# Kernel optimization log

Hardware: AMD Instinct MI355X
Metric: run time of the kernel (lower is better)

The kernel has to match this reference:

```python
import jax, jax.numpy as jnp
import numpy as np

N, E = 50000, 800000
IN, H, D = 64, 4, 16          # in_feats, num_heads, head_size (IN == H*D -> identity skip)
NT, ET = 2, 2                 # num node / edge types


def setup_inputs() -> dict:
    key = jax.random.key(0)
    ks = jax.random.split(key, 13)
    s = 0.05
    return {
        "x": jax.random.normal(ks[0], (N, IN), jnp.float32),
        # TypedLinear weights: one [in,out] matrix per node type (DGL TypedLinear, no bias)
        "Wk": jax.random.normal(ks[1], (NT, IN, H * D), jnp.float32) * s,
        "Wq": jax.random.normal(ks[2], (NT, IN, H * D), jnp.float32) * s,
        "Wv": jax.random.normal(ks[3], (NT, IN, H * D), jnp.float32) * s,
        "Wa": jax.random.normal(ks[4], (NT, H * D, H * D), jnp.float32) * s,
        # per-head, per-edge-type relation matrices (relation_att / relation_msg)
        "Ratt": jax.random.normal(ks[5], (H, ET, D, D), jnp.float32) * s,
        "Rmsg": jax.random.normal(ks[6], (H, ET, D, D), jnp.float32) * s,
        "pri": jnp.ones((H, ET), jnp.float32),   # relation_pri
        "skip": jnp.ones((NT,), jnp.float32),    # skip gate per node type
        "ntype": jax.random.randint(ks[7], (N,), 0, NT),
        "etype": jax.random.randint(ks[8], (E,), 0, ET),
        "src": jax.random.randint(ks[9], (E,), 0, N),
        "dst": jax.random.randint(ks[10], (E,), 0, N),
    }


def _typed_linear(x, W, types):
    # x:[N,I], W:[T,I,O], types:[N] -> y[n] = x[n] @ W[types[n]]
    # T is tiny (2): compute all types densely, then select per node.
    y_all = jnp.einsum('ni,tio->tno', x, W)
    return y_all[types, jnp.arange(x.shape[0])]


def reference(x, Wk, Wq, Wv, Wa, Ratt, Rmsg, pri, skip, ntype, etype, src, dst):
    n = x.shape[0]
    k = _typed_linear(x, Wk, ntype).reshape(n, H, D)
    q = _typed_linear(x, Wq, ntype).reshape(n, H, D)
    v = _typed_linear(x, Wv, ntype).reshape(n, H, D)
    # relation transforms per edge type, computed once at node level (ET is tiny),
    # then gathered per edge: equivalent to per-edge TypedLinear in DGL's message fn.
    katt = jnp.einsum('nhd,htdf->thnf', k, Ratt)   # [ET,H,N,D]
    vmsg = jnp.einsum('nhd,htdf->thnf', v, Rmsg)   # [ET,H,N,D]
    kw = katt[etype, :, src]                       # [E,H,D]
    m = vmsg[etype, :, src]                        # [E,H,D]
    qd = q[dst]                                    # [E,H,D]
    # attention logits: (K W_att) . Q * relation_pri / sqrt(d)
    a = (kw * qd).sum(-1) * pri[:, etype].T / jnp.sqrt(jnp.float32(D))  # [E,H]
    # edge softmax over incoming edges of each destination node (stable)
    amax = jax.ops.segment_max(a, dst, num_segments=n)                  # [N,H]
    ae = jnp.exp(a - amax[dst])
    asum = jax.ops.segment_sum(ae, dst, num_segments=n)
    attn = ae / asum[dst]                                               # [E,H]
    # scatter-aggregate messages
    h = jax.ops.segment_sum(m * attn[:, :, None], dst, num_segments=n)  # [N,H,D]
    # target-specific output projection (dropout is identity in eval)
    h = _typed_linear(h.reshape(n, H * D), Wa, ntype)                   # [N,H*D]
    # sigmoid-gated skip (in_feats == H*D so identity residual)
    alpha = jax.nn.sigmoid(skip)[ntype][:, None]
    return h * alpha + x * (1.0 - alpha)
```

## Files before the change

kernel.cpp:

```cpp
#include <hip/hip_runtime.h>
#include <math.h>
#include <stdint.h>

#define N_NODES 50000
#define N_EDGES 800000
#define NT_TYPES 2
#define ET_TYPES 2
#define NB_SCAN ((N_NODES + 255) / 256)
#define M_COLS 320
#define M_PER_T (64 * M_COLS)
#define PROJ_GRID ((N_NODES + 63) / 64)
#define SCAT_GRID ((N_EDGES + 1023) / 1024)
#define AGG_GRID ((N_NODES + 15) / 16)
#define MAXDEG 64
#define LOG2E 1.44269504088896f
#define HSTRIDE 36

typedef __attribute__((ext_vector_type(8))) short short8v;
typedef __attribute__((ext_vector_type(4))) float float4v;

__device__ __forceinline__ unsigned int f32_to_bf16(float f) {
  unsigned int u = __float_as_uint(f);
  return (u + 0x7FFFu + ((u >> 16) & 1u)) >> 16;
}

__device__ __forceinline__ float row16_sum(float p) {
  int r;
  r = __builtin_amdgcn_update_dpp(0, __float_as_int(p), 0x128, 0xf, 0xf, false);
  p += __int_as_float(r);
  r = __builtin_amdgcn_update_dpp(0, __float_as_int(p), 0x124, 0xf, 0xf, false);
  p += __int_as_float(r);
  r = __builtin_amdgcn_update_dpp(0, __float_as_int(p), 0x122, 0xf, 0xf, false);
  p += __int_as_float(r);
  r = __builtin_amdgcn_update_dpp(0, __float_as_int(p), 0x121, 0xf, 0xf, false);
  p += __int_as_float(r);
  return p;
}

__global__ void zero_kernel(int* __restrict__ deg) {
  const int i = blockIdx.x * 256 + threadIdx.x;
  if (i < N_NODES + 2) deg[i] = 0;
}

__global__ void prep_kernel(
    const float* __restrict__ Wk, const float* __restrict__ Wq,
    const float* __restrict__ Wv, const float* __restrict__ Wa,
    const float* __restrict__ Ratt, const float* __restrict__ Rmsg,
    const float* __restrict__ pri, const int* __restrict__ ntype,
    unsigned short* __restrict__ M2b, unsigned short* __restrict__ Wa2b,
    int* __restrict__ tcnt, int* __restrict__ tlist) {
  const int idx = blockIdx.x * 256 + threadIdx.x;
  if (idx < NT_TYPES * 4096) {
    int t = idx >> 12;
    int rem = idx & 4095;
    int col = rem >> 6, k = rem & 63;
    Wa2b[idx] = (unsigned short)f32_to_bf16(Wa[(size_t)t * 4096 + k * 64 + col]);
  }
  if (idx < NT_TYPES * M_PER_T) {
    int t = idx / M_PER_T;
    int rem = idx % M_PER_T;
    int col = rem / 64;
    int k = rem % 64;
    float val;
    if (col < 64) {
      val = Wq[(size_t)t * 4096 + k * 64 + col];
    } else {
      int cc = col - 64;
      int et = cc >> 7;
      int r = cc & 127;
      int c = r >> 1;
      int half = r & 1;
      int h = c >> 4, f = c & 15;
      const float* W = half ? Wv : Wk;
      const float* R = half ? Rmsg : Ratt;
      float s = 0.f;
#pragma unroll
      for (int d = 0; d < 16; ++d)
        s = fmaf(W[(size_t)t * 4096 + k * 64 + h * 16 + d],
                 R[(((size_t)h * ET_TYPES + et) * 16 + d) * 16 + f], s);
      if (half == 0) s *= pri[h * ET_TYPES + et] * 0.25f * LOG2E;
      val = s;
    }
    M2b[idx] = (unsigned short)f32_to_bf16(val);
  }
  {
    __shared__ int lcnt[NT_TYPES];
    __shared__ int lbase[NT_TYPES];
    if (threadIdx.x < NT_TYPES) lcnt[threadIdx.x] = 0;
    __syncthreads();
    int t = 0, lpos = 0;
    const bool valid = (idx < N_NODES);
    if (valid) {
      t = ntype[idx];
      lpos = atomicAdd(&lcnt[t], 1);
    }
    __syncthreads();
    if (threadIdx.x < NT_TYPES)
      lbase[threadIdx.x] = atomicAdd(&tcnt[threadIdx.x], lcnt[threadIdx.x]);
    __syncthreads();
    if (valid)
      tlist[t * N_NODES + lbase[t] + lpos] = idx;
  }
}

__global__ __launch_bounds__(256) void projscatter_kernel(
    const float* __restrict__ x,
    const unsigned short* __restrict__ M2b,
    const int* __restrict__ tcnt, const int* __restrict__ tlist,
    unsigned short* __restrict__ qb, unsigned int* __restrict__ kvb,
    const int* __restrict__ src, const int* __restrict__ dst,
    const int* __restrict__ etype, int* __restrict__ deg,
    int* __restrict__ csr) {
  const int bid = blockIdx.x;
  if (bid >= 2 * PROJ_GRID) {
    const int ebase = (bid - 2 * PROJ_GRID) * 1024 + threadIdx.x;
    int dsts[4], recs[4];
#pragma unroll
    for (int k = 0; k < 4; ++k) {
      int e = ebase + k * 256;
      bool v = (e < N_EDGES);
      dsts[k] = v ? dst[e] : -1;
      recs[k] = v ? ((etype[e] * N_NODES + src[e]) << 6) : 0;
    }
#pragma unroll
    for (int k = 0; k < 4; ++k) {
      if (dsts[k] >= 0) {
        int r = atomicAdd(&deg[dsts[k]], 1);
        __builtin_nontemporal_store(recs[k], &csr[(dsts[k] << 6) + r]);
      }
    }
    return;
  }
  const int ty = bid & 1;
  const int pb = bid >> 1;
  const int wave = threadIdx.x >> 6;
  const int lane = threadIdx.x & 63;
  const int cnt = __builtin_amdgcn_readfirstlane(tcnt[ty]);
  const int base = (pb * 4 + wave) * 16;
  if (base >= cnt) return;

  const int* lst = tlist + ty * N_NODES;
  const int l15 = lane & 15;
  const int lq = lane >> 4;

  const int nidA = lst[min(base + l15, cnt - 1)];
  const float4* xr = reinterpret_cast<const float4*>(x + (size_t)nidA * 64);
  const float4 xa0 = xr[lq * 2 + 0];
  const float4 xa1 = xr[lq * 2 + 1];
  const float4 xb0 = xr[8 + lq * 2 + 0];
  const float4 xb1 = xr[8 + lq * 2 + 1];
  union { short8v v; unsigned int u[4]; } A0u, A1u;
  A0u.u[0] = f32_to_bf16(xa0.x) | (f32_to_bf16(xa0.y) << 16);
  A0u.u[1] = f32_to_bf16(xa0.z) | (f32_to_bf16(xa0.w) << 16);
  A0u.u[2] = f32_to_bf16(xa1.x) | (f32_to_bf16(xa1.y) << 16);
  A0u.u[3] = f32_to_bf16(xa1.z) | (f32_to_bf16(xa1.w) << 16);
  A1u.u[0] = f32_to_bf16(xb0.x) | (f32_to_bf16(xb0.y) << 16);
  A1u.u[1] = f32_to_bf16(xb0.z) | (f32_to_bf16(xb0.w) << 16);
  A1u.u[2] = f32_to_bf16(xb1.x) | (f32_to_bf16(xb1.y) << 16);
  A1u.u[3] = f32_to_bf16(xb1.z) | (f32_to_bf16(xb1.w) << 16);
  const short8v A0 = A0u.v;
  const short8v A1 = A1u.v;

  const int n0 = lst[min(base + lq * 4 + 0, cnt - 1)];
  const int n1 = lst[min(base + lq * 4 + 1, cnt - 1)];
  const int n2 = lst[min(base + lq * 4 + 2, cnt - 1)];
  const int n3 = lst[min(base + lq * 4 + 3, cnt - 1)];

  const unsigned short* Bb = M2b + (size_t)ty * M_PER_T;

#pragma unroll
  for (int ct = 0; ct < 20; ++ct) {
    const int colb = ct * 16 + l15;
    const short8v B0 = *reinterpret_cast<const short8v*>(
        Bb + (size_t)colb * 64 + lq * 8);
    const short8v B1 = *reinterpret_cast<const short8v*>(
        Bb + (size_t)colb * 64 + 32 + lq * 8);
    float4v C = {0.f, 0.f, 0.f, 0.f};
    C = __builtin_amdgcn_mfma_f32_16x16x32_bf16(A0, B0, C, 0, 0, 0);
    C = __builtin_amdgcn_mfma_f32_16x16x32_bf16(A1, B1, C, 0, 0, 0);

    if (ct < 4) {
      qb[(size_t)n0 * 64 + colb] = (unsigned short)f32_to_bf16(C[0]);
      qb[(size_t)n1 * 64 + colb] = (unsigned short)f32_to_bf16(C[1]);
      qb[(size_t)n2 * 64 + colb] = (unsigned short)f32_to_bf16(C[2]);
      qb[(size_t)n3 * 64 + colb] = (unsigned short)f32_to_bf16(C[3]);
    } else {
      const float p0 = __shfl_xor(C[0], 1, 64);
      const float p1 = __shfl_xor(C[1], 1, 64);
      const float p2 = __shfl_xor(C[2], 1, 64);
      const float p3 = __shfl_xor(C[3], 1, 64);
      if ((lane & 1) == 0) {
        const int cc = colb - 64;
        const int et = cc >> 7;
        const int c = (cc & 127) >> 1;
        const size_t b0 = ((size_t)et * N_NODES) * 64 + c;
        kvb[b0 + (size_t)n0 * 64] = f32_to_bf16(C[0]) | (f32_to_bf16(p0) << 16);
        kvb[b0 + (size_t)n1 * 64] = f32_to_bf16(C[1]) | (f32_to_bf16(p1) << 16);
        kvb[b0 + (size_t)n2 * 64] = f32_to_bf16(C[2]) | (f32_to_bf16(p2) << 16);
        kvb[b0 + (size_t)n3 * 64] = f32_to_bf16(C[3]) | (f32_to_bf16(p3) << 16);
      }
    }
  }
}

__device__ __forceinline__ void edge_update(unsigned int wrd, float qd,
                                            float& srun, float& acc) {
  float kw = __uint_as_float(wrd << 16);
  float mv = __uint_as_float(wrd & 0xFFFF0000u);
  float w = __builtin_amdgcn_exp2f(row16_sum(kw * qd));
  srun += w;
  acc = fmaf(mv, w, acc);
}

__global__ __launch_bounds__(256) void agg_out_kernel(
    const unsigned short* __restrict__ qb, const unsigned int* __restrict__ kvb,
    const int* __restrict__ deg, const int* __restrict__ csr,
    const unsigned short* __restrict__ Wa2b, const float* __restrict__ x,
    const float* __restrict__ skip, const int* __restrict__ tcnt,
    const int* __restrict__ tlist, float* __restrict__ out) {
  __shared__ unsigned int hlds[16 * HSTRIDE];
  const int wave = threadIdx.x >> 6;
  const int lane = threadIdx.x & 63;
  const int ty = blockIdx.y;
  const int cnt = __builtin_amdgcn_readfirstlane(tcnt[ty]);
  const int base = blockIdx.x * 16;
  if (base >= cnt) return;
  const int* lst = tlist + ty * N_NODES;

  for (int half = 0; half < 2; ++half) {
    const int lrowA = wave * 4 + half * 2;
    int nA = __builtin_amdgcn_readfirstlane(lst[min(base + lrowA, cnt - 1)]);
    int nB = __builtin_amdgcn_readfirstlane(lst[min(base + lrowA + 1, cnt - 1)]);
    const float qdA = __uint_as_float((unsigned int)qb[(size_t)nA * 64 + lane] << 16);
    const float qdB = __uint_as_float((unsigned int)qb[(size_t)nB * 64 + lane] << 16);
    const int eA = __builtin_amdgcn_readfirstlane(deg[nA]);
    const int eB = __builtin_amdgcn_readfirstlane(deg[nB]);
    const int* cA = csr + (nA << 6);
    const int* cB = csr + (nB << 6);

    float sA = 0.f, aA = 0.f, sB = 0.f, aB = 0.f;
    const int m = min(eA, eB);
    int j = 0;
    for (; j + 4 <= m; j += 4) {
      int pA0 = __builtin_amdgcn_readfirstlane(cA[j + 0]);
      int pA1 = __builtin_amdgcn_readfirstlane(cA[j + 1]);
      int pA2 = __builtin_amdgcn_readfirstlane(cA[j + 2]);
      int pA3 = __builtin_amdgcn_readfirstlane(cA[j + 3]);
      int pB0 = __builtin_amdgcn_readfirstlane(cB[j + 0]);
      int pB1 = __builtin_amdgcn_readfirstlane(cB[j + 1]);
      int pB2 = __builtin_amdgcn_readfirstlane(cB[j + 2]);
      int pB3 = __builtin_amdgcn_readfirstlane(cB[j + 3]);
      unsigned int wA0 = kvb[(unsigned)pA0 + lane];
      unsigned int wA1 = kvb[(unsigned)pA1 + lane];
      unsigned int wA2 = kvb[(unsigned)pA2 + lane];
      unsigned int wA3 = kvb[(unsigned)pA3 + lane];
      unsigned int wB0 = kvb[(unsigned)pB0 + lane];
      unsigned int wB1 = kvb[(unsigned)pB1 + lane];
      unsigned int wB2 = kvb[(unsigned)pB2 + lane];
      unsigned int wB3 = kvb[(unsigned)pB3 + lane];
      edge_update(wA0, qdA, sA, aA);
      edge_update(wB0, qdB, sB, aB);
      edge_update(wA1, qdA, sA, aA);
      edge_update(wB1, qdB, sB, aB);
      edge_update(wA2, qdA, sA, aA);
      edge_update(wB2, qdB, sB, aB);
      edge_update(wA3, qdA, sA, aA);
      edge_update(wB3, qdB, sB, aB);
    }
    int jA = j;
    for (; jA + 4 <= eA; jA += 4) {
      int p0 = __builtin_amdgcn_readfirstlane(cA[jA + 0]);
      int p1 = __builtin_amdgcn_readfirstlane(cA[jA + 1]);
      int p2 = __builtin_amdgcn_readfirstlane(cA[jA + 2]);
      int p3 = __builtin_amdgcn_readfirstlane(cA[jA + 3]);
      unsigned int w0 = kvb[(unsigned)p0 + lane];
      unsigned int w1 = kvb[(unsigned)p1 + lane];
      unsigned int w2 = kvb[(unsigned)p2 + lane];
      unsigned int w3 = kvb[(unsigned)p3 + lane];
      edge_update(w0, qdA, sA, aA);
      edge_update(w1, qdA, sA, aA);
      edge_update(w2, qdA, sA, aA);
      edge_update(w3, qdA, sA, aA);
    }
    for (; jA < eA; ++jA) {
      int p = __builtin_amdgcn_readfirstlane(cA[jA]);
      edge_update(kvb[(unsigned)p + lane], qdA, sA, aA);
    }
    int jB = j;
    for (; jB + 4 <= eB; jB += 4) {
      int p0 = __builtin_amdgcn_readfirstlane(cB[jB + 0]);
      int p1 = __builtin_amdgcn_readfirstlane(cB[jB + 1]);
      int p2 = __builtin_amdgcn_readfirstlane(cB[jB + 2]);
      int p3 = __builtin_amdgcn_readfirstlane(cB[jB + 3]);
      unsigned int w0 = kvb[(unsigned)p0 + lane];
      unsigned int w1 = kvb[(unsigned)p1 + lane];
      unsigned int w2 = kvb[(unsigned)p2 + lane];
      unsigned int w3 = kvb[(unsigned)p3 + lane];
      edge_update(w0, qdB, sB, aB);
      edge_update(w1, qdB, sB, aB);
      edge_update(w2, qdB, sB, aB);
      edge_update(w3, qdB, sB, aB);
    }
    for (; jB < eB; ++jB) {
      int p = __builtin_amdgcn_readfirstlane(cB[jB]);
      edge_update(kvb[(unsigned)p + lane], qdB, sB, aB);
    }

    float hvA = (sA > 0.f) ? (aA / sA) : 0.f;
    float hvB = (sB > 0.f) ? (aB / sB) : 0.f;
    float prA = __shfl_xor(hvA, 1, 64);
    float prB = __shfl_xor(hvB, 1, 64);
    if ((lane & 1) == 0) {
      hlds[lrowA * HSTRIDE + (lane >> 1)] =
          f32_to_bf16(hvA) | (f32_to_bf16(prA) << 16);
      hlds[(lrowA + 1) * HSTRIDE + (lane >> 1)] =
          f32_to_bf16(hvB) | (f32_to_bf16(prB) << 16);
    }
  }
  __syncthreads();

  const int l15 = lane & 15;
  const int lq = lane >> 4;
  const short8v A0 = *reinterpret_cast<const short8v*>(&hlds[l15 * HSTRIDE + lq * 4]);
  const short8v A1 = *reinterpret_cast<const short8v*>(&hlds[l15 * HSTRIDE + 16 + lq * 4]);

  const int n0 = lst[min(base + lq * 4 + 0, cnt - 1)];
  const int n1 = lst[min(base + lq * 4 + 1, cnt - 1)];
  const int n2 = lst[min(base + lq * 4 + 2, cnt - 1)];
  const int n3 = lst[min(base + lq * 4 + 3, cnt - 1)];

  const float alpha = 1.f / (1.f + __expf(-skip[ty]));
  const float beta = 1.f - alpha;
  const unsigned short* Bb = Wa2b + (size_t)ty * 4096;

  const int colb = wave * 16 + l15;
  const short8v B0 = *reinterpret_cast<const short8v*>(
      Bb + (size_t)colb * 64 + lq * 8);
  const short8v B1 = *reinterpret_cast<const short8v*>(
      Bb + (size_t)colb * 64 + 32 + lq * 8);
  float4v C = {0.f, 0.f, 0.f, 0.f};
  C = __builtin_amdgcn_mfma_f32_16x16x32_bf16(A0, B0, C, 0, 0, 0);
  C = __builtin_amdgcn_mfma_f32_16x16x32_bf16(A1, B1, C, 0, 0, 0);

  const size_t o0 = (size_t)n0 * 64 + colb;
  const size_t o1 = (size_t)n1 * 64 + colb;
  const size_t o2 = (size_t)n2 * 64 + colb;
  const size_t o3 = (size_t)n3 * 64 + colb;
  out[o0] = C[0] * alpha + x[o0] * beta;
  out[o1] = C[1] * alpha + x[o1] * beta;
  out[o2] = C[2] * alpha + x[o2] * beta;
  out[o3] = C[3] * alpha + x[o3] * beta;
}

extern "C" void kernel_launch(void* const* d_in, const int* in_sizes, int n_in,
                              void* d_out, int out_size, void* d_ws, size_t ws_size,
                              hipStream_t stream) {
  const float* x    = (const float*)d_in[0];
  const float* Wk   = (const float*)d_in[1];
  const float* Wq   = (const float*)d_in[2];
  const float* Wv   = (const float*)d_in[3];
  const float* Wa   = (const float*)d_in[4];
  const float* Ratt = (const float*)d_in[5];
  const float* Rmsg = (const float*)d_in[6];
  const float* pri  = (const float*)d_in[7];
  const float* skip = (const float*)d_in[8];
  const int* ntype  = (const int*)d_in[9];
  const int* etype  = (const int*)d_in[10];
  const int* src    = (const int*)d_in[11];
  const int* dst    = (const int*)d_in[12];
  float* out = (float*)d_out;

  unsigned short* qb = (unsigned short*)d_ws;
  unsigned int* kvb = (unsigned int*)(qb + (size_t)N_NODES * 64);
  int* deg   = (int*)(kvb + (size_t)ET_TYPES * N_NODES * 64);
  int* tcnt  = deg + N_NODES;
  int* tlist = tcnt + 2;
  int* csr   = tlist + 2 * N_NODES;
  unsigned short* M2b = (unsigned short*)
      (((uintptr_t)(csr + (size_t)N_NODES * MAXDEG) + 255) & ~(uintptr_t)255);
  unsigned short* Wa2b = (unsigned short*)
      (((uintptr_t)(M2b + NT_TYPES * M_PER_T) + 255) & ~(uintptr_t)255);

  zero_kernel<<<NB_SCAN, 256, 0, stream>>>(deg);

  prep_kernel<<<NB_SCAN, 256, 0, stream>>>(
      Wk, Wq, Wv, Wa, Ratt, Rmsg, pri, ntype, M2b, Wa2b, tcnt, tlist);

  projscatter_kernel<<<2 * PROJ_GRID + SCAT_GRID, 256, 0, stream>>>(
      x, M2b, tcnt, tlist, qb, kvb, src, dst, etype, deg, csr);

  dim3 agrid(AGG_GRID, NT_TYPES);
  agg_out_kernel<<<agrid, 256, 0, stream>>>(
      qb, (const unsigned int*)kvb, deg, csr, Wa2b, x, skip, tcnt, tlist, out);
}
```

Baseline: 115.9 us.

## Drop per-type node bucketing; compute both type projections and select per row

Removes the zero kernel and the ntype bucketing (tlist/tcnt). Zeroing of deg is folded into prep_kernel. The projection and output kernels now process nodes in natural order, run the MFMAs for both node-type weight matrices and select the result per row by ntype. The edge scatter is also split to one edge per thread. This saves a launch, the atomics, and the indirect list lookups, which also makes node accesses contiguous. In exchange it doubles the MFMA and weight-load work.

New measurement: 102.0 us. 1.14x faster.

```diff
diff --git a/kernel.cpp b/kernel.cpp
--- a/kernel.cpp
+++ b/kernel.cpp
@@ -10,8 +10,8 @@
 #define M_COLS 320
 #define M_PER_T (64 * M_COLS)
 #define PROJ_GRID ((N_NODES + 63) / 64)
-#define SCAT_GRID ((N_EDGES + 1023) / 1024)
-#define AGG_GRID ((N_NODES + 15) / 16)
+#define SCAT_GRID ((N_EDGES + 255) / 256)
+#define AGG_GRID (N_NODES / 16)
 #define MAXDEG 64
 #define LOG2E 1.44269504088896f
 #define HSTRIDE 36
@@ -37,19 +37,15 @@
   return p;
 }
 
-__global__ void zero_kernel(int* __restrict__ deg) {
-  const int i = blockIdx.x * 256 + threadIdx.x;
-  if (i < N_NODES + 2) deg[i] = 0;
-}
-
 __global__ void prep_kernel(
     const float* __restrict__ Wk, const float* __restrict__ Wq,
     const float* __restrict__ Wv, const float* __restrict__ Wa,
     const float* __restrict__ Ratt, const float* __restrict__ Rmsg,
-    const float* __restrict__ pri, const int* __restrict__ ntype,
+    const float* __restrict__ pri,
     unsigned short* __restrict__ M2b, unsigned short* __restrict__ Wa2b,
-    int* __restrict__ tcnt, int* __restrict__ tlist) {
+    int* __restrict__ deg) {
   const int idx = blockIdx.x * 256 + threadIdx.x;
+  if (idx < N_NODES) deg[idx] = 0;
   if (idx < NT_TYPES * 4096) {
     int t = idx >> 12;
     int rem = idx & 4095;
@@ -83,67 +79,34 @@
     }
     M2b[idx] = (unsigned short)f32_to_bf16(val);
   }
-  {
-    __shared__ int lcnt[NT_TYPES];
-    __shared__ int lbase[NT_TYPES];
-    if (threadIdx.x < NT_TYPES) lcnt[threadIdx.x] = 0;
-    __syncthreads();
-    int t = 0, lpos = 0;
-    const bool valid = (idx < N_NODES);
-    if (valid) {
-      t = ntype[idx];
-      lpos = atomicAdd(&lcnt[t], 1);
-    }
-    __syncthreads();
-    if (threadIdx.x < NT_TYPES)
-      lbase[threadIdx.x] = atomicAdd(&tcnt[threadIdx.x], lcnt[threadIdx.x]);
-    __syncthreads();
-    if (valid)
-      tlist[t * N_NODES + lbase[t] + lpos] = idx;
-  }
 }
 
 __global__ __launch_bounds__(256) void projscatter_kernel(
     const float* __restrict__ x,
     const unsigned short* __restrict__ M2b,
-    const int* __restrict__ tcnt, const int* __restrict__ tlist,
+    const int* __restrict__ ntype,
     unsigned short* __restrict__ qb, unsigned int* __restrict__ kvb,
     const int* __restrict__ src, const int* __restrict__ dst,
     const int* __restrict__ etype, int* __restrict__ deg,
     int* __restrict__ csr) {
   const int bid = blockIdx.x;
-  if (bid >= 2 * PROJ_GRID) {
-    const int ebase = (bid - 2 * PROJ_GRID) * 1024 + threadIdx.x;
-    int dsts[4], recs[4];
-#pragma unroll
-    for (int k = 0; k < 4; ++k) {
-      int e = ebase + k * 256;
-      bool v = (e < N_EDGES);
-      dsts[k] = v ? dst[e] : -1;
-      recs[k] = v ? ((etype[e] * N_NODES + src[e]) << 6) : 0;
-    }
-#pragma unroll
-    for (int k = 0; k < 4; ++k) {
-      if (dsts[k] >= 0) {
-        int r = atomicAdd(&deg[dsts[k]], 1);
-        __builtin_nontemporal_store(recs[k], &csr[(dsts[k] << 6) + r]);
-      }
+  if (bid >= PROJ_GRID) {
+    const int e = (bid - PROJ_GRID) * 256 + threadIdx.x;
+    if (e < N_EDGES) {
+      int d = dst[e];
+      int r = atomicAdd(&deg[d], 1);
+      __builtin_nontemporal_store((etype[e] * N_NODES + src[e]) << 6,
+                                  &csr[(d << 6) + r]);
     }
     return;
   }
-  const int ty = bid & 1;
-  const int pb = bid >> 1;
   const int wave = threadIdx.x >> 6;
   const int lane = threadIdx.x & 63;
-  const int cnt = __builtin_amdgcn_readfirstlane(tcnt[ty]);
-  const int base = (pb * 4 + wave) * 16;
-  if (base >= cnt) return;
-
-  const int* lst = tlist + ty * N_NODES;
+  const int base = bid * 64 + wave * 16;
   const int l15 = lane & 15;
   const int lq = lane >> 4;
 
-  const int nidA = lst[min(base + l15, cnt - 1)];
+  const int nidA = min(base + l15, N_NODES - 1);
   const float4* xr = reinterpret_cast<const float4*>(x + (size_t)nidA * 64);
   const float4 xa0 = xr[lq * 2 + 0];
   const float4 xa1 = xr[lq * 2 + 1];
@@ -161,43 +124,51 @@
   const short8v A0 = A0u.v;
   const short8v A1 = A1u.v;
 
-  const int n0 = lst[min(base + lq * 4 + 0, cnt - 1)];
-  const int n1 = lst[min(base + lq * 4 + 1, cnt - 1)];
-  const int n2 = lst[min(base + lq * 4 + 2, cnt - 1)];
-  const int n3 = lst[min(base + lq * 4 + 3, cnt - 1)];
-
-  const unsigned short* Bb = M2b + (size_t)ty * M_PER_T;
+  const int n0 = min(base + lq * 4 + 0, N_NODES - 1);
+  const int n1 = min(base + lq * 4 + 1, N_NODES - 1);
+  const int n2 = min(base + lq * 4 + 2, N_NODES - 1);
+  const int n3 = min(base + lq * 4 + 3, N_NODES - 1);
+  const int t0 = ntype[n0], t1 = ntype[n1], t2 = ntype[n2], t3 = ntype[n3];
 
 #pragma unroll
   for (int ct = 0; ct < 20; ++ct) {
     const int colb = ct * 16 + l15;
-    const short8v B0 = *reinterpret_cast<const short8v*>(
-        Bb + (size_t)colb * 64 + lq * 8);
-    const short8v B1 = *reinterpret_cast<const short8v*>(
-        Bb + (size_t)colb * 64 + 32 + lq * 8);
-    float4v C = {0.f, 0.f, 0.f, 0.f};
-    C = __builtin_amdgcn_mfma_f32_16x16x32_bf16(A0, B0, C, 0, 0, 0);
-    C = __builtin_amdgcn_mfma_f32_16x16x32_bf16(A1, B1, C, 0, 0, 0);
+    const size_t boff = (size_t)colb * 64 + lq * 8;
+    const short8v B00 = *reinterpret_cast<const short8v*>(M2b + boff);
+    const short8v B01 = *reinterpret_cast<const short8v*>(M2b + boff + 32);
+    const short8v B10 = *reinterpret_cast<const short8v*>(M2b + M_PER_T + boff);
+    const short8v B11 = *reinterpret_cast<const short8v*>(M2b + M_PER_T + boff + 32);
+    float4v C0 = {0.f, 0.f, 0.f, 0.f};
+    C0 = __builtin_amdgcn_mfma_f32_16x16x32_bf16(A0, B00, C0, 0, 0, 0);
+    C0 = __builtin_amdgcn_mfma_f32_16x16x32_bf16(A1, B01, C0, 0, 0, 0);
+    float4v C1 = {0.f, 0.f, 0.f, 0.f};
+    C1 = __builtin_amdgcn_mfma_f32_16x16x32_bf16(A0, B10, C1, 0, 0, 0);
+    C1 = __builtin_amdgcn_mfma_f32_16x16x32_bf16(A1, B11, C1, 0, 0, 0);
+
+    const float v0 = t0 ? C1[0] : C0[0];
+    const float v1 = t1 ? C1[1] : C0[1];
+    const float v2 = t2 ? C1[2] : C0[2];
+    const float v3 = t3 ? C1[3] : C0[3];
 
     if (ct < 4) {
-      qb[(size_t)n0 * 64 + colb] = (unsigned short)f32_to_bf16(C[0]);
-      qb[(size_t)n1 * 64 + colb] = (unsigned short)f32_to_bf16(C[1]);
-      qb[(size_t)n2 * 64 + colb] = (unsigned short)f32_to_bf16(C[2]);
-      qb[(size_t)n3 * 64 + colb] = (unsigned short)f32_to_bf16(C[3]);
+      qb[(size_t)n0 * 64 + colb] = (unsigned short)f32_to_bf16(v0);
+      qb[(size_t)n1 * 64 + colb] = (unsigned short)f32_to_bf16(v1);
+      qb[(size_t)n2 * 64 + colb] = (unsigned short)f32_to_bf16(v2);
+      qb[(size_t)n3 * 64 + colb] = (unsigned short)f32_to_bf16(v3);
     } else {
-      const float p0 = __shfl_xor(C[0], 1, 64);
-      const float p1 = __shfl_xor(C[1], 1, 64);
-      const float p2 = __shfl_xor(C[2], 1, 64);
-      const float p3 = __shfl_xor(C[3], 1, 64);
+      const float p0 = __shfl_xor(v0, 1, 64);
+      const float p1 = __shfl_xor(v1, 1, 64);
+      const float p2 = __shfl_xor(v2, 1, 64);
+      const float p3 = __shfl_xor(v3, 1, 64);
       if ((lane & 1) == 0) {
         const int cc = colb - 64;
         const int et = cc >> 7;
         const int c = (cc & 127) >> 1;
         const size_t b0 = ((size_t)et * N_NODES) * 64 + c;
-        kvb[b0 + (size_t)n0 * 64] = f32_to_bf16(C[0]) | (f32_to_bf16(p0) << 16);
-        kvb[b0 + (size_t)n1 * 64] = f32_to_bf16(C[1]) | (f32_to_bf16(p1) << 16);
-        kvb[b0 + (size_t)n2 * 64] = f32_to_bf16(C[2]) | (f32_to_bf16(p2) << 16);
-        kvb[b0 + (size_t)n3 * 64] = f32_to_bf16(C[3]) | (f32_to_bf16(p3) << 16);
+        kvb[b0 + (size_t)n0 * 64] = f32_to_bf16(v0) | (f32_to_bf16(p0) << 16);
+        kvb[b0 + (size_t)n1 * 64] = f32_to_bf16(v1) | (f32_to_bf16(p1) << 16);
+        kvb[b0 + (size_t)n2 * 64] = f32_to_bf16(v2) | (f32_to_bf16(p2) << 16);
+        kvb[b0 + (size_t)n3 * 64] = f32_to_bf16(v3) | (f32_to_bf16(p3) << 16);
       }
     }
   }
@@ -216,21 +187,17 @@
     const unsigned short* __restrict__ qb, const unsigned int* __restrict__ kvb,
     const int* __restrict__ deg, const int* __restrict__ csr,
     const unsigned short* __restrict__ Wa2b, const float* __restrict__ x,
-    const float* __restrict__ skip, const int* __restrict__ tcnt,
-    const int* __restrict__ tlist, float* __restrict__ out) {
+    const float* __restrict__ skip, const int* __restrict__ ntype,
+    float* __restrict__ out) {
   __shared__ unsigned int hlds[16 * HSTRIDE];
   const int wave = threadIdx.x >> 6;
   const int lane = threadIdx.x & 63;
-  const int ty = blockIdx.y;
-  const int cnt = __builtin_amdgcn_readfirstlane(tcnt[ty]);
   const int base = blockIdx.x * 16;
-  if (base >= cnt) return;
-  const int* lst = tlist + ty * N_NODES;
 
   for (int half = 0; half < 2; ++half) {
     const int lrowA = wave * 4 + half * 2;
-    int nA = __builtin_amdgcn_readfirstlane(lst[min(base + lrowA, cnt - 1)]);
-    int nB = __builtin_amdgcn_readfirstlane(lst[min(base + lrowA + 1, cnt - 1)]);
+    const int nA = __builtin_amdgcn_readfirstlane(base + lrowA);
+    const int nB = __builtin_amdgcn_readfirstlane(base + lrowA + 1);
     const float qdA = __uint_as_float((unsigned int)qb[(size_t)nA * 64 + lane] << 16);
     const float qdB = __uint_as_float((unsigned int)qb[(size_t)nB * 64 + lane] << 16);
     const int eA = __builtin_amdgcn_readfirstlane(deg[nA]);
@@ -324,32 +291,45 @@
   const short8v A0 = *reinterpret_cast<const short8v*>(&hlds[l15 * HSTRIDE + lq * 4]);
   const short8v A1 = *reinterpret_cast<const short8v*>(&hlds[l15 * HSTRIDE + 16 + lq * 4]);
 
-  const int n0 = lst[min(base + lq * 4 + 0, cnt - 1)];
-  const int n1 = lst[min(base + lq * 4 + 1, cnt - 1)];
-  const int n2 = lst[min(base + lq * 4 + 2, cnt - 1)];
-  const int n3 = lst[min(base + lq * 4 + 3, cnt - 1)];
-
-  const float alpha = 1.f / (1.f + __expf(-skip[ty]));
-  const float beta = 1.f - alpha;
-  const unsigned short* Bb = Wa2b + (size_t)ty * 4096;
+  const int n0 = base + lq * 4 + 0;
+  const int n1 = base + lq * 4 + 1;
+  const int n2 = base + lq * 4 + 2;
+  const int n3 = base + lq * 4 + 3;
+  const int t0 = ntype[n0], t1 = ntype[n1], t2 = ntype[n2], t3 = ntype[n3];
+
+  const float alpha0 = 1.f / (1.f + __expf(-skip[0]));
+  const float alpha1 = 1.f / (1.f + __expf(-skip[1]));
 
   const int colb = wave * 16 + l15;
-  const short8v B0 = *reinterpret_cast<const short8v*>(
-      Bb + (size_t)colb * 64 + lq * 8);
-  const short8v B1 = *reinterpret_cast<const short8v*>(
-      Bb + (size_t)colb * 64 + 32 + lq * 8);
-  float4v C = {0.f, 0.f, 0.f, 0.f};
-  C = __builtin_amdgcn_mfma_f32_16x16x32_bf16(A0, B0, C, 0, 0, 0);
-  C = __builtin_amdgcn_mfma_f32_16x16x32_bf16(A1, B1, C, 0, 0, 0);
+  const size_t boff = (size_t)colb * 64 + lq * 8;
+  const short8v B00 = *reinterpret_cast<const short8v*>(Wa2b + boff);
+  const short8v B01 = *reinterpret_cast<const short8v*>(Wa2b + boff + 32);
+  const short8v B10 = *reinterpret_cast<const short8v*>(Wa2b + 4096 + boff);
+  const short8v B11 = *reinterpret_cast<const short8v*>(Wa2b + 4096 + boff + 32);
+  float4v C0 = {0.f, 0.f, 0.f, 0.f};
+  C0 = __builtin_amdgcn_mfma_f32_16x16x32_bf16(A0, B00, C0, 0, 0, 0);
+  C0 = __builtin_amdgcn_mfma_f32_16x16x32_bf16(A1, B01, C0, 0, 0, 0);
+  float4v C1 = {0.f, 0.f, 0.f, 0.f};
+  C1 = __builtin_amdgcn_mfma_f32_16x16x32_bf16(A0, B10, C1, 0, 0, 0);
+  C1 = __builtin_amdgcn_mfma_f32_16x16x32_bf16(A1, B11, C1, 0, 0, 0);
+
+  const float al0 = t0 ? alpha1 : alpha0;
+  const float al1 = t1 ? alpha1 : alpha0;
+  const float al2 = t2 ? alpha1 : alpha0;
+  const float al3 = t3 ? alpha1 : alpha0;
+  const float v0 = t0 ? C1[0] : C0[0];
+  const float v1 = t1 ? C1[1] : C0[1];
+  const float v2 = t2 ? C1[2] : C0[2];
+  const float v3 = t3 ? C1[3] : C0[3];
 
   const size_t o0 = (size_t)n0 * 64 + colb;
   const size_t o1 = (size_t)n1 * 64 + colb;
   const size_t o2 = (size_t)n2 * 64 + colb;
   const size_t o3 = (size_t)n3 * 64 + colb;
-  out[o0] = C[0] * alpha + x[o0] * beta;
-  out[o1] = C[1] * alpha + x[o1] * beta;
-  out[o2] = C[2] * alpha + x[o2] * beta;
-  out[o3] = C[3] * alpha + x[o3] * beta;
+  out[o0] = v0 * al0 + x[o0] * (1.f - al0);
+  out[o1] = v1 * al1 + x[o1] * (1.f - al1);
+  out[o2] = v2 * al2 + x[o2] * (1.f - al2);
+  out[o3] = v3 * al3 + x[o3] * (1.f - al3);
 }
 
 extern "C" void kernel_launch(void* const* d_in, const int* in_sizes, int n_in,
@@ -372,24 +352,19 @@
 
   unsigned short* qb = (unsigned short*)d_ws;
   unsigned int* kvb = (unsigned int*)(qb + (size_t)N_NODES * 64);
-  int* deg   = (int*)(kvb + (size_t)ET_TYPES * N_NODES * 64);
-  int* tcnt  = deg + N_NODES;
-  int* tlist = tcnt + 2;
-  int* csr   = tlist + 2 * N_NODES;
+  int* deg = (int*)(kvb + (size_t)ET_TYPES * N_NODES * 64);
+  int* csr = deg + N_NODES;
   unsigned short* M2b = (unsigned short*)
       (((uintptr_t)(csr + (size_t)N_NODES * MAXDEG) + 255) & ~(uintptr_t)255);
   unsigned short* Wa2b = (unsigned short*)
       (((uintptr_t)(M2b + NT_TYPES * M_PER_T) + 255) & ~(uintptr_t)255);
 
-  zero_kernel<<<NB_SCAN, 256, 0, stream>>>(deg);
-
   prep_kernel<<<NB_SCAN, 256, 0, stream>>>(
-      Wk, Wq, Wv, Wa, Ratt, Rmsg, pri, ntype, M2b, Wa2b, tcnt, tlist);
-
-  projscatter_kernel<<<2 * PROJ_GRID + SCAT_GRID, 256, 0, stream>>>(
-      x, M2b, tcnt, tlist, qb, kvb, src, dst, etype, deg, csr);
-
-  dim3 agrid(AGG_GRID, NT_TYPES);
-  agg_out_kernel<<<agrid, 256, 0, stream>>>(
-      qb, (const unsigned int*)kvb, deg, csr, Wa2b, x, skip, tcnt, tlist, out);
-}
+      Wk, Wq, Wv, Wa, Ratt, Rmsg, pri, M2b, Wa2b, deg);
+
+  projscatter_kernel<<<PROJ_GRID + SCAT_GRID, 256, 0, stream>>>(
+      x, M2b, ntype, qb, kvb, src, dst, etype, deg, csr);
+
+  agg_out_kernel<<<AGG_GRID, 256, 0, stream>>>(
+      qb, (const unsigned int*)kvb, deg, csr, Wa2b, x, skip, ntype, out);
+}
```
